# Performance work log

Hardware: AMD Instinct MI355X
Metric: run time of the kernel (lower is better)

The kernel has to match this reference:

```python
import jax, jax.numpy as jnp
from jax import lax
import numpy as np

V, E, H = 32000, 32, 8  # vocab, embed dim, hidden dim
S, B = 128, 64          # seq_len, batch


def setup_inputs() -> dict:
    key = jax.random.key(0)
    ks = jax.random.split(key, 16)
    u = lambda k, shape, s: jax.random.uniform(k, shape, jnp.float32, -s, s)
    sH = 1.0 / np.sqrt(H)
    sE = 1.0 / np.sqrt(E)
    sV = 1.0 / np.sqrt(V)
    return {
        "input_batch": jax.random.randint(ks[0], (S, B), 0, V),
        "lookup": u(ks[1], (V, E), sE),
        "weight_xf": u(ks[2], (E, H), sH),
        "weight_hf": u(ks[3], (H, H), sH),
        "weight_xb": u(ks[4], (E, H), sH),
        "weight_hb": u(ks[5], (H, H), sH),
        "weight_o": u(ks[6], (2 * H, V), sV),
        "H_f": u(ks[7], (H,), sH),
        "H_b": u(ks[8], (H,), sH),
        "b_f1": u(ks[9], (H,), sH),
        "b_f2": u(ks[10], (H,), sH),
        "b_b1": u(ks[11], (H,), sH),
        "b_b2": u(ks[12], (H,), sH),
        "b_o": u(ks[13], (V,), sV),
    }


def reference(input_batch, lookup, weight_xf, weight_hf, weight_xb, weight_hb,
              weight_o, H_f, H_b, b_f1, b_f2, b_b1, b_b2, b_o):
    seq, bsz = input_batch.shape
    X = lookup[input_batch]  # [S, B, E]

    # NOTE: the torch code stores the hidden state BEFORE consuming token i
    # (H_f_table[i] = Hf_pre), so scan emits the carry before the update.
    def step_f(h, x):
        h_new = jnp.tanh(x @ weight_xf + b_f1 + h @ weight_hf + b_f2)
        return h_new, h

    def step_b(h, x):
        h_new = jnp.tanh(x @ weight_xb + b_b1 + h @ weight_hb + b_b2)
        return h_new, h

    h0f = jnp.broadcast_to(H_f, (bsz, H))
    h0b = jnp.broadcast_to(H_b, (bsz, H))
    _, Hf_table = lax.scan(step_f, h0f, X)            # [S, B, H] (pre-states)
    _, Hb_rev = lax.scan(step_b, h0b, X[::-1])        # reversed pre-states
    Hb_table = Hb_rev[::-1]                           # [S, B, H]

    Hcat = jnp.concatenate([Hf_table, Hb_table], axis=-1)   # [S, B, 2H]
    logits = jnp.einsum('sbh,hv->sbv', Hcat, weight_o) + b_o
    return jax.nn.log_softmax(logits, axis=-1)
```

## Files before the change

kernel.cpp:

```cpp
#include <hip/hip_runtime.h>

#define SEQ 128
#define BSZ 64
#define EMB 32
#define HD  8
#define VOC 32000
#define NPOS (SEQ * BSZ)
#define NRB  (NPOS / 32)
#define NVS  40
#define TPW  25
#define LOG2E 1.4426950408889634f

typedef float f32x4  __attribute__((ext_vector_type(4)));
typedef short bf16x8 __attribute__((ext_vector_type(8)));
typedef float f32x16 __attribute__((ext_vector_type(16)));

__device__ __forceinline__ unsigned short f2bf(float f) {
    union { float f; unsigned int u; } x; x.f = f;
    unsigned int r = x.u + 0x7fffu + ((x.u >> 16) & 1u);
    return (unsigned short)(r >> 16);
}

__global__ __launch_bounds__(256) void prep_kernel(
    const int*   __restrict__ idx,
    const float* __restrict__ lookup,
    const float* __restrict__ Wxf, const float* __restrict__ Wxb,
    const float* __restrict__ bf1, const float* __restrict__ bf2,
    const float* __restrict__ bb1, const float* __restrict__ bb2,
    const float* __restrict__ Wo,  const float* __restrict__ bo,
    float* __restrict__ xpf, float* __restrict__ xpb,
    unsigned short* __restrict__ wt, unsigned short* __restrict__ wt2,
    float* __restrict__ bo2)
{
    if (blockIdx.x < 32) {
        const int i = blockIdx.x * 256 + threadIdx.x;
        const int s = i >> 6;
        const int b = i & 63;

        const float* xr = lookup + (size_t)idx[i] * EMB;
        float x[EMB];
#pragma unroll
        for (int e = 0; e < EMB; ++e) x[e] = xr[e];

#pragma unroll
        for (int h = 0; h < HD; ++h) {
            float af = bf1[h] + bf2[h];
            float ab = bb1[h] + bb2[h];
#pragma unroll
            for (int e = 0; e < EMB; ++e) {
                af = fmaf(x[e], Wxf[e * HD + h], af);
                ab = fmaf(x[e], Wxb[e * HD + h], ab);
            }
            xpf[(b * HD + h) * SEQ + s]             = af;
            xpb[(b * HD + h) * SEQ + (SEQ - 1 - s)] = ab;
        }
    } else {
        const int v = (blockIdx.x - 32) * 256 + threadIdx.x;
        if (v < VOC) {
#pragma unroll
            for (int k = 0; k < 16; ++k) {
                const float w = Wo[k * VOC + v];
                wt [v * 16 + k] = f2bf(w);
                wt2[v * 16 + k] = f2bf(w * LOG2E);
            }
            bo2[v] = bo[v] * LOG2E;
        }
    }
}

__global__ __launch_bounds__(512) void rnn_scan_kernel(
    const float* __restrict__ xpf, const float* __restrict__ xpb,
    const float* __restrict__ Whf, const float* __restrict__ Whb,
    const float* __restrict__ Hf0, const float* __restrict__ Hb0,
    unsigned short* __restrict__ hc2)
{
    const int dir = blockIdx.x;
    const int tid = threadIdx.x;
    const int b   = tid >> 3;
    const int h   = tid & 7;

    const float* Wh = dir ? Whb : Whf;
    const float* xp = (dir ? xpb : xpf) + (size_t)tid * SEQ;

    float wh[HD];
#pragma unroll
    for (int j = 0; j < HD; ++j) wh[j] = Wh[j * HD + h];

    float xs[SEQ];
    const f32x4* xp4 = (const f32x4*)xp;
#pragma unroll
    for (int q = 0; q < SEQ / 4; ++q) {
        f32x4 v = xp4[q];
        xs[4 * q + 0] = v.x; xs[4 * q + 1] = v.y;
        xs[4 * q + 2] = v.z; xs[4 * q + 3] = v.w;
    }

    float hcur = dir ? Hb0[h] : Hf0[h];
    const int koff = dir ? HD : 0;

#pragma unroll
    for (int t = 0; t < SEQ; ++t) {
        const int s = dir ? (SEQ - 1 - t) : t;
        hc2[(s * BSZ + b) * 16 + koff + h] = f2bf(hcur);

        float acc = xs[t];
#pragma unroll
        for (int j = 0; j < HD; ++j)
            acc = fmaf(__shfl(hcur, j, 8), wh[j], acc);

        float e = __expf(2.0f * acc);
        hcur = (e - 1.0f) / (e + 1.0f);
    }
}

__global__ __launch_bounds__(256) void lse_partial_kernel(
    const unsigned short* __restrict__ hc2,
    const unsigned short* __restrict__ wt2,
    const float* __restrict__ bo2,
    float* __restrict__ partial)
{
    const int gw   = blockIdx.x * 4 + (threadIdx.x >> 6);
    const int rb   = gw / NVS;
    const int vs   = gw - rb * NVS;
    const int lane = threadIdx.x & 63;
    const int half = lane >> 5;
    const int lc   = lane & 31;

    const bf16x8 afrag = *(const bf16x8*)(hc2 + (size_t)(rb * 32 + lc) * 16 + half * 8);

    f32x16 zv;
#pragma unroll
    for (int i = 0; i < 16; ++i) zv[i] = 0.0f;

    float sacc[16];
#pragma unroll
    for (int g = 0; g < 16; ++g) sacc[g] = 0.0f;

    for (int t = 0; t < TPW; ++t) {
        const int v0 = (vs * TPW + t) * 32;
        const bf16x8 bfrag = *(const bf16x8*)(wt2 + (size_t)(v0 + lc) * 16 + half * 8);
        f32x16 d = __builtin_amdgcn_mfma_f32_32x32x16_bf16(afrag, bfrag, zv, 0, 0, 0);
        const float bov = bo2[v0 + lc];
#pragma unroll
        for (int g = 0; g < 16; ++g)
            sacc[g] += exp2f(d[g] + bov);
    }

#pragma unroll
    for (int g = 0; g < 16; ++g) {
        float s = sacc[g];
        s += __shfl_xor(s, 1, 32);
        s += __shfl_xor(s, 2, 32);
        s += __shfl_xor(s, 4, 32);
        s += __shfl_xor(s, 8, 32);
        s += __shfl_xor(s, 16, 32);
        sacc[g] = s;
    }

    if (lc == 0) {
#pragma unroll
        for (int g = 0; g < 16; ++g) {
            const int row = (g & 3) + 8 * (g >> 2) + 4 * half;
            partial[(size_t)(rb * 32 + row) * NVS + vs] = sacc[g];
        }
    }
}

__global__ __launch_bounds__(256) void out_mfma_kernel(
    const unsigned short* __restrict__ hc2,
    const unsigned short* __restrict__ wt,
    const float* __restrict__ bo,
    const float* __restrict__ partial,
    float* __restrict__ out)
{
    const int gw   = blockIdx.x * 4 + (threadIdx.x >> 6);
    const int rb   = gw / NVS;
    const int vs   = gw - rb * NVS;
    const int lane = threadIdx.x & 63;
    const int half = lane >> 5;
    const int lc   = lane & 31;

    const float* pbase = partial + (size_t)rb * 32 * NVS
                       + (lane >> 1) * NVS + (lane & 1) * (NVS / 2);
    float s = 0.0f;
    const f32x4* p4 = (const f32x4*)pbase;
#pragma unroll
    for (int q = 0; q < NVS / 8; ++q) {
        f32x4 v = p4[q];
        s += v.x + v.y + v.z + v.w;
    }
    s += __shfl_xor(s, 1, 64);

    float lse16[16];
#pragma unroll
    for (int g = 0; g < 16; ++g) {
        const int row = (g & 3) + 8 * (g >> 2) + 4 * half;
        lse16[g] = logf(__shfl(s, 2 * row, 64));
    }

    const bf16x8 afrag = *(const bf16x8*)(hc2 + (size_t)(rb * 32 + lc) * 16 + half * 8);

    f32x16 zv;
#pragma unroll
    for (int i = 0; i < 16; ++i) zv[i] = 0.0f;

    for (int t = 0; t < TPW; ++t) {
        const int v0 = (vs * TPW + t) * 32;
        const bf16x8 bfrag = *(const bf16x8*)(wt + (size_t)(v0 + lc) * 16 + half * 8);
        f32x16 d = __builtin_amdgcn_mfma_f32_32x32x16_bf16(afrag, bfrag, zv, 0, 0, 0);
        const float bov = bo[v0 + lc];
#pragma unroll
        for (int g = 0; g < 16; ++g) {
            const int row = (g & 3) + 8 * (g >> 2) + 4 * half;
            const float val = d[g] + bov - lse16[g];
            __builtin_nontemporal_store(
                val, out + (size_t)(rb * 32 + row) * VOC + v0 + lc);
        }
    }
}

extern "C" void kernel_launch(void* const* d_in, const int* in_sizes, int n_in,
                              void* d_out, int out_size, void* d_ws, size_t ws_size,
                              hipStream_t stream)
{
    const int*   idx    = (const int*)  d_in[0];
    const float* lookup = (const float*)d_in[1];
    const float* Wxf    = (const float*)d_in[2];
    const float* Whf    = (const float*)d_in[3];
    const float* Wxb    = (const float*)d_in[4];
    const float* Whb    = (const float*)d_in[5];
    const float* Wo     = (const float*)d_in[6];
    const float* Hf0    = (const float*)d_in[7];
    const float* Hb0    = (const float*)d_in[8];
    const float* bf1    = (const float*)d_in[9];
    const float* bf2    = (const float*)d_in[10];
    const float* bb1    = (const float*)d_in[11];
    const float* bb2    = (const float*)d_in[12];
    const float* bo     = (const float*)d_in[13];
    float* out = (float*)d_out;

    char* ws = (char*)d_ws;
    float*          xpf     = (float*)ws;          ws += BSZ * HD * SEQ * 4;
    float*          xpb     = (float*)ws;          ws += BSZ * HD * SEQ * 4;
    unsigned short* hc2     = (unsigned short*)ws; ws += NPOS * 16 * 2;
    unsigned short* wt      = (unsigned short*)ws; ws += VOC * 16 * 2;
    unsigned short* wt2     = (unsigned short*)ws; ws += VOC * 16 * 2;
    float*          bo2     = (float*)ws;          ws += VOC * 4;
    float*          partial = (float*)ws;          ws += (size_t)NPOS * NVS * 4;

    hipLaunchKernelGGL(prep_kernel, dim3(32 + (VOC + 255) / 256), dim3(256), 0, stream,
                       idx, lookup, Wxf, Wxb, bf1, bf2, bb1, bb2, Wo, bo,
                       xpf, xpb, wt, wt2, bo2);
    hipLaunchKernelGGL(rnn_scan_kernel, dim3(2), dim3(512), 0, stream,
                       xpf, xpb, Whf, Whb, Hf0, Hb0, hc2);
    hipLaunchKernelGGL(lse_partial_kernel, dim3(NRB * NVS / 4), dim3(256), 0, stream,
                       hc2, wt2, bo2, partial);
    hipLaunchKernelGGL(out_mfma_kernel, dim3(NRB * NVS / 4), dim3(256), 0, stream,
                       hc2, wt, bo, partial, out);
}
```

Baseline: 314.8 us.

## Fuse log-sum-exp partial and output kernels into one block-per-rowblock kernel

Merges the separate partial-sum and output kernels into one kernel. Each block owns a 32-row block, and its 8 waves split the vocabulary between them. Per-row exp sums are reduced through LDS, and the output pass then reuses the log2e-scaled bf16 weights with a LN2 rescale, which removes the unscaled weight copy, the partial buffer round-trip and one launch. In exchange the grid shrinks from ~10K small blocks to 256 blocks of 512 threads, which may lower occupancy and the latency hiding for the write-bound output stores. Reusing the scaled bf16 weights also changes rounding slightly.

```diff
diff --git a/kernel.cpp b/kernel.cpp
--- a/kernel.cpp
+++ b/kernel.cpp
@@ -7,9 +7,10 @@
 #define VOC 32000
 #define NPOS (SEQ * BSZ)
 #define NRB  (NPOS / 32)
-#define NVS  40
-#define TPW  25
+#define NTILE (VOC / 32)
+#define TPW  (NTILE / 8)
 #define LOG2E 1.4426950408889634f
+#define LN2   0.6931471805599453f
 
 typedef float f32x4  __attribute__((ext_vector_type(4)));
 typedef short bf16x8 __attribute__((ext_vector_type(8)));
@@ -29,8 +30,7 @@
     const float* __restrict__ bb1, const float* __restrict__ bb2,
     const float* __restrict__ Wo,  const float* __restrict__ bo,
     float* __restrict__ xpf, float* __restrict__ xpb,
-    unsigned short* __restrict__ wt, unsigned short* __restrict__ wt2,
-    float* __restrict__ bo2)
+    unsigned short* __restrict__ wt2, float* __restrict__ bo2)
 {
     if (blockIdx.x < 32) {
         const int i = blockIdx.x * 256 + threadIdx.x;
@@ -58,11 +58,8 @@
         const int v = (blockIdx.x - 32) * 256 + threadIdx.x;
         if (v < VOC) {
 #pragma unroll
-            for (int k = 0; k < 16; ++k) {
-                const float w = Wo[k * VOC + v];
-                wt [v * 16 + k] = f2bf(w);
-                wt2[v * 16 + k] = f2bf(w * LOG2E);
-            }
+            for (int k = 0; k < 16; ++k)
+                wt2[v * 16 + k] = f2bf(Wo[k * VOC + v] * LOG2E);
             bo2[v] = bo[v] * LOG2E;
         }
     }
@@ -113,18 +110,21 @@
     }
 }
 
-__global__ __launch_bounds__(256) void lse_partial_kernel(
+__global__ __launch_bounds__(512) void fused_out_kernel(
     const unsigned short* __restrict__ hc2,
     const unsigned short* __restrict__ wt2,
     const float* __restrict__ bo2,
-    float* __restrict__ partial)
-{
-    const int gw   = blockIdx.x * 4 + (threadIdx.x >> 6);
-    const int rb   = gw / NVS;
-    const int vs   = gw - rb * NVS;
-    const int lane = threadIdx.x & 63;
+    float* __restrict__ out)
+{
+    __shared__ float lds_sum[8][32];
+    __shared__ float lds_lse[32];
+
+    const int tid  = threadIdx.x;
+    const int w    = tid >> 6;
+    const int lane = tid & 63;
     const int half = lane >> 5;
     const int lc   = lane & 31;
+    const int rb   = blockIdx.x;
 
     const bf16x8 afrag = *(const bf16x8*)(hc2 + (size_t)(rb * 32 + lc) * 16 + half * 8);
 
@@ -136,8 +136,9 @@
 #pragma unroll
     for (int g = 0; g < 16; ++g) sacc[g] = 0.0f;
 
+#pragma unroll 2
     for (int t = 0; t < TPW; ++t) {
-        const int v0 = (vs * TPW + t) * 32;
+        const int v0 = (w * TPW + t) * 32;
         const bf16x8 bfrag = *(const bf16x8*)(wt2 + (size_t)(v0 + lc) * 16 + half * 8);
         f32x16 d = __builtin_amdgcn_mfma_f32_32x32x16_bf16(afrag, bfrag, zv, 0, 0, 0);
         const float bov = bo2[v0 + lc];
@@ -156,63 +157,40 @@
         s += __shfl_xor(s, 16, 32);
         sacc[g] = s;
     }
-
     if (lc == 0) {
 #pragma unroll
         for (int g = 0; g < 16; ++g) {
             const int row = (g & 3) + 8 * (g >> 2) + 4 * half;
-            partial[(size_t)(rb * 32 + row) * NVS + vs] = sacc[g];
-        }
-    }
-}
-
-__global__ __launch_bounds__(256) void out_mfma_kernel(
-    const unsigned short* __restrict__ hc2,
-    const unsigned short* __restrict__ wt,
-    const float* __restrict__ bo,
-    const float* __restrict__ partial,
-    float* __restrict__ out)
-{
-    const int gw   = blockIdx.x * 4 + (threadIdx.x >> 6);
-    const int rb   = gw / NVS;
-    const int vs   = gw - rb * NVS;
-    const int lane = threadIdx.x & 63;
-    const int half = lane >> 5;
-    const int lc   = lane & 31;
-
-    const float* pbase = partial + (size_t)rb * 32 * NVS
-                       + (lane >> 1) * NVS + (lane & 1) * (NVS / 2);
-    float s = 0.0f;
-    const f32x4* p4 = (const f32x4*)pbase;
-#pragma unroll
-    for (int q = 0; q < NVS / 8; ++q) {
-        f32x4 v = p4[q];
-        s += v.x + v.y + v.z + v.w;
-    }
-    s += __shfl_xor(s, 1, 64);
-
-    float lse16[16];
+            lds_sum[w][row] = sacc[g];
+        }
+    }
+    __syncthreads();
+
+    if (tid < 32) {
+        float s = 0.0f;
+#pragma unroll
+        for (int ww = 0; ww < 8; ++ww) s += lds_sum[ww][tid];
+        lds_lse[tid] = logf(s);
+    }
+    __syncthreads();
+
+    float nls[16];
 #pragma unroll
     for (int g = 0; g < 16; ++g) {
         const int row = (g & 3) + 8 * (g >> 2) + 4 * half;
-        lse16[g] = logf(__shfl(s, 2 * row, 64));
-    }
-
-    const bf16x8 afrag = *(const bf16x8*)(hc2 + (size_t)(rb * 32 + lc) * 16 + half * 8);
-
-    f32x16 zv;
-#pragma unroll
-    for (int i = 0; i < 16; ++i) zv[i] = 0.0f;
-
+        nls[g] = -lds_lse[row];
+    }
+
+#pragma unroll 2
     for (int t = 0; t < TPW; ++t) {
-        const int v0 = (vs * TPW + t) * 32;
-        const bf16x8 bfrag = *(const bf16x8*)(wt + (size_t)(v0 + lc) * 16 + half * 8);
+        const int v0 = (w * TPW + t) * 32;
+        const bf16x8 bfrag = *(const bf16x8*)(wt2 + (size_t)(v0 + lc) * 16 + half * 8);
         f32x16 d = __builtin_amdgcn_mfma_f32_32x32x16_bf16(afrag, bfrag, zv, 0, 0, 0);
-        const float bov = bo[v0 + lc];
+        const float bov = bo2[v0 + lc];
 #pragma unroll
         for (int g = 0; g < 16; ++g) {
             const int row = (g & 3) + 8 * (g >> 2) + 4 * half;
-            const float val = d[g] + bov - lse16[g];
+            const float val = fmaf(d[g] + bov, LN2, nls[g]);
             __builtin_nontemporal_store(
                 val, out + (size_t)(rb * 32 + row) * VOC + v0 + lc);
         }
@@ -240,21 +218,17 @@
     float* out = (float*)d_out;
 
     char* ws = (char*)d_ws;
-    float*          xpf     = (float*)ws;          ws += BSZ * HD * SEQ * 4;
-    float*          xpb     = (float*)ws;          ws += BSZ * HD * SEQ * 4;
-    unsigned short* hc2     = (unsigned short*)ws; ws += NPOS * 16 * 2;
-    unsigned short* wt      = (unsigned short*)ws; ws += VOC * 16 * 2;
-    unsigned short* wt2     = (unsigned short*)ws; ws += VOC * 16 * 2;
-    float*          bo2     = (float*)ws;          ws += VOC * 4;
-    float*          partial = (float*)ws;          ws += (size_t)NPOS * NVS * 4;
-
-    hipLaunchKernelGGL(prep_kernel, dim3(32 + (VOC + 255) / 256), dim3(256), 0, stream,
+    float*          xpf = (float*)ws;          ws += BSZ * HD * SEQ * 4;
+    float*          xpb = (float*)ws;          ws += BSZ * HD * SEQ * 4;
+    unsigned short* hc2 = (unsigned short*)ws; ws += NPOS * 16 * 2;
+    unsigned short* wt2 = (unsigned short*)ws; ws += VOC * 16 * 2;
+    float*          bo2 = (float*)ws;          ws += VOC * 4;
+
+    hipLaunchKernelGGL(prep_kernel, dim3(32 + VOC / 256), dim3(256), 0, stream,
                        idx, lookup, Wxf, Wxb, bf1, bf2, bb1, bb2, Wo, bo,
-                       xpf, xpb, wt, wt2, bo2);
+                       xpf, xpb, wt2, bo2);
     hipLaunchKernelGGL(rnn_scan_kernel, dim3(2), dim3(512), 0, stream,
                        xpf, xpb, Whf, Whb, Hf0, Hb0, hc2);
-    hipLaunchKernelGGL(lse_partial_kernel, dim3(NRB * NVS / 4), dim3(256), 0, stream,
-                       hc2, wt2, bo2, partial);
-    hipLaunchKernelGGL(out_mfma_kernel, dim3(NRB * NVS / 4), dim3(256), 0, stream,
-                       hc2, wt, bo, partial, out);
-}
+    hipLaunchKernelGGL(fused_out_kernel, dim3(NRB), dim3(512), 0, stream,
+                       hc2, wt2, bo2, out);
+}
```

Result: slower. 416.1 us (+32.2%).
